# Optimization experiments

Hardware: AMD Instinct MI355X
Metric: run time of the kernel (lower is better)

## Reference

```python
import jax, jax.numpy as jnp
import numpy as np
import math

N_HEAD = 16
STRIDE = 128
C = 8


def _sparse_causal_mask(q_len, k_len):
    # Mirrors LingLongAttention._sparse_causal_mask (static, host-side numpy).
    cols = np.arange(k_len)
    rows = np.arange(k_len)[:, None]
    strided = (cols % STRIDE) >= (STRIDE - C)          # last C cols of each stride block
    local = (cols[None, :] // STRIDE) == (rows // STRIDE)  # same stride block as query
    causal = cols[None, :] <= rows
    layout = (strided[None, :] | local) & causal       # [k_len, k_len]
    return jnp.asarray(layout[k_len - q_len:])         # [q_len, k_len]


def setup_inputs() -> dict:
    key = jax.random.key(0)
    k1, k2, k3 = jax.random.split(key, 3)
    B, S, E = 2, 2048, 1024
    return {
        "hidden_states": jax.random.normal(k1, (B, S, E), dtype=jnp.float32),
        "W_attn": jax.random.normal(k2, (E, 3 * E), dtype=jnp.float32) * 0.02,
        "b_attn": jnp.zeros((3 * E,), dtype=jnp.float32),
        "W_proj": jax.random.normal(k3, (E, E), dtype=jnp.float32) * 0.02,
        "b_proj": jnp.zeros((E,), dtype=jnp.float32),
    }


def reference(hidden_states, W_attn, b_attn, W_proj, b_proj):
    B, S, E = hidden_states.shape
    H = N_HEAD
    D = E // H
    # Conv1D: x @ W + b, then split into q,k,v
    qkv = hidden_states @ W_attn + b_attn                 # [B,S,3E]
    q, k, v = jnp.split(qkv, 3, axis=-1)
    split = lambda t: t.reshape(B, S, H, D).transpose(0, 2, 1, 3)  # [B,H,S,D]
    q, k, v = split(q), split(k), split(v)
    scale = jnp.asarray(1.0 / math.sqrt(D), dtype=q.dtype)
    scores = jnp.einsum("bhqd,bhkd->bhqk", q, k) * scale  # [B,H,S,S]
    mask = _sparse_causal_mask(S, S)[None, None]          # [1,1,S,S]
    mask_value = jnp.asarray(jnp.finfo(scores.dtype).min, dtype=scores.dtype)
    scores = jnp.where(mask, scores, mask_value)
    attn = jax.nn.softmax(scores, axis=-1)
    out = jnp.einsum("bhqk,bhkd->bhqd", attn, v)          # [B,H,S,D]
    out = out.transpose(0, 2, 1, 3).reshape(B, S, E)      # merge heads
    return out @ W_proj + b_proj
```

## Files before the change

kernel.cpp:

```cpp
#include <hip/hip_runtime.h>
#include <hip/hip_bf16.h>
#include <stdint.h>

typedef unsigned short u16;
typedef uint32_t u32;
typedef short s16x8 __attribute__((ext_vector_type(8)));
typedef float f32x4 __attribute__((ext_vector_type(4)));

#define SDIM 2048
#define EDIM 1024

static __device__ __forceinline__ float b2f(u16 v) {
    union { float f; u32 u; } c; c.u = ((u32)v) << 16; return c.f;
}
static __device__ __forceinline__ u16 f2b(float f) {
    union { float f; u32 u; } c; c.f = f;
    u32 u = c.u;
    u32 r = (u + 0x7FFFu + ((u >> 16) & 1u)) >> 16;
    return (u16)r;
}
static __device__ __forceinline__ void gll16(const u16* g, u16* l) {
    __builtin_amdgcn_global_load_lds(
        (const __attribute__((address_space(1))) void*)g,
        (__attribute__((address_space(3))) void*)l, 16, 0, 0);
}

static __device__ __forceinline__ int sniff_bf16(const u16* __restrict__ x) {
    u16 v = x[(threadIdx.x & 63) * 2];
    int e = (v >> 7) & 0xFF;
    unsigned long long m = __ballot(e >= 90 && e <= 144);
    return __popcll(m) >= 48;
}

__global__ __launch_bounds__(256) void k_prep(
    const void* __restrict__ X, const void* __restrict__ Wa,
    const void* __restrict__ Wp, u16* __restrict__ Xb,
    u16* __restrict__ WtA, u16* __restrict__ WtP) {
    int f = sniff_bf16((const u16*)X);
    int z = blockIdx.z;
    int t = threadIdx.x;
    if (z == 2) {
        if (f) return;
        const float* s = (const float*)X;
        int bid = blockIdx.y * 48 + blockIdx.x;
        for (int c = bid; c < 2048; c += 768) {
            long i = ((long)c * 256 + t) * 8;
            u16 o[8];
            for (int j = 0; j < 8; ++j) o[j] = f2b(s[i + j]);
            *(uint4*)&Xb[i] = *(uint4*)o;
        }
        return;
    }
    if (z == 1 && blockIdx.x >= 16) return;
    const void* src = z ? Wp : Wa;
    u16* dst = z ? WtP : WtA;
    int Nsrc = z ? 1024 : 3072;
    int n0 = blockIdx.x * 64, k0 = blockIdx.y * 64;
    __shared__ u16 L[64 * 72];
    int r = t >> 2, c0 = (t & 3) * 16;
    u16 val[16];
    if (f) {
        const u16* s = (const u16*)src + (size_t)(k0 + r) * Nsrc + n0 + c0;
        *(uint4*)&val[0] = *(const uint4*)s;
        *(uint4*)&val[8] = *(const uint4*)(s + 8);
    } else {
        const float* s = (const float*)src + (size_t)(k0 + r) * Nsrc + n0 + c0;
        for (int j = 0; j < 16; ++j) val[j] = f2b(s[j]);
    }
    for (int j = 0; j < 16; ++j) L[(c0 + j) * 72 + r] = val[j];
    __syncthreads();
    uint4 o0 = *(const uint4*)&L[r * 72 + c0];
    uint4 o1 = *(const uint4*)&L[r * 72 + c0 + 8];
    u16* d = dst + (size_t)(n0 + r) * 1024 + k0 + c0;
    *(uint4*)d = o0;
    *(uint4*)(d + 8) = o1;
}

__global__ __launch_bounds__(256) void k_gemm1(
    const u16* __restrict__ Xraw, const u16* __restrict__ Xb,
    const u16* __restrict__ Bt, const void* __restrict__ bias,
    u16* __restrict__ C) {
    const int K = 1024;
    __shared__ u16 As[3][4096];
    __shared__ u16 Bs[3][4096];
    int f = sniff_bf16(Xraw);
    const u16* A = f ? Xraw : Xb;
    int t = threadIdx.x, wave = t >> 6, lane = t & 63;
    int m0 = blockIdx.y * 128, n0 = blockIdx.x * 128;
    int wm = (wave >> 1) * 64, wn = (wave & 1) * 64;
    int lm = lane & 15;
    int lk = (((lane >> 4) ^ ((lane >> 1) & 3))) * 8;
    int sr = t >> 2;
    int sc = ((t & 3) ^ ((t >> 3) & 3)) * 8;
    const u16* Ap = A + (size_t)(m0 + sr) * K + sc;
    const u16* Bp = Bt + (size_t)(n0 + sr) * K + sc;
    int wo = wave * 512;

    f32x4 acc[4][4];
    f32x4 z = {0.f, 0.f, 0.f, 0.f};
    for (int mi = 0; mi < 4; ++mi)
        for (int ni = 0; ni < 4; ++ni) acc[mi][ni] = z;

    gll16(Ap, &As[0][wo]);
    gll16(Ap + (size_t)64 * K, &As[0][wo + 2048]);
    gll16(Bp, &Bs[0][wo]);
    gll16(Bp + (size_t)64 * K, &Bs[0][wo + 2048]);
    gll16(Ap + 32, &As[1][wo]);
    gll16(Ap + (size_t)64 * K + 32, &As[1][wo + 2048]);
    gll16(Bp + 32, &Bs[1][wo]);
    gll16(Bp + (size_t)64 * K + 32, &Bs[1][wo + 2048]);

    u16 *Ac = &As[0][0], *An = &As[1][0], *At = &As[2][0];
    u16 *Bc = &Bs[0][0], *Bn = &Bs[1][0], *Btg = &Bs[2][0];

    for (int it = 0; it < 32; ++it) {
        asm volatile("s_waitcnt vmcnt(4)\n\ts_barrier" ::: "memory");
        int kn = ((it + 2) & 31) * 32;
        gll16(Ap + kn, At + wo);
        gll16(Ap + (size_t)64 * K + kn, At + wo + 2048);
        gll16(Bp + kn, Btg + wo);
        gll16(Bp + (size_t)64 * K + kn, Btg + wo + 2048);

        s16x8 af[4], bfr[4];
        for (int mi = 0; mi < 4; ++mi)
            af[mi] = *(const s16x8*)&Ac[(wm + mi * 16 + lm) * 32 + lk];
        for (int ni = 0; ni < 4; ++ni)
            bfr[ni] = *(const s16x8*)&Bc[(wn + ni * 16 + lm) * 32 + lk];
        for (int mi = 0; mi < 4; ++mi)
            for (int ni = 0; ni < 4; ++ni)
                acc[mi][ni] = __builtin_amdgcn_mfma_f32_16x16x32_bf16(
                    af[mi], bfr[ni], acc[mi][ni], 0, 0, 0);

        u16* tp = Ac; Ac = An; An = At; At = tp;
        tp = Bc; Bc = Bn; Bn = Btg; Btg = tp;
    }
    asm volatile("s_waitcnt vmcnt(0)" ::: "memory");

    int cn = lane & 15, cr = (lane >> 4) * 4;
    for (int ni = 0; ni < 4; ++ni) {
        int gn = n0 + wn + ni * 16 + cn;
        float bb = f ? b2f(((const u16*)bias)[gn]) : ((const float*)bias)[gn];
        int kind = gn >> 10, rem = gn & 1023;
        int h = rem >> 6, d = rem & 63;
        int hm = kind * 32 + h;
        for (int mi = 0; mi < 4; ++mi)
            for (int r = 0; r < 4; ++r) {
                int gm = m0 + wm + mi * 16 + cr + r;
                int b = gm >> 11, s = gm & 2047;
                size_t o = ((size_t)((hm + b * 16) * 2048 + s)) * 64 + d;
                C[o] = f2b(acc[mi][ni][r] + bb);
            }
    }
}

__global__ __launch_bounds__(256) void k_gemm2(
    const u16* __restrict__ Xraw, const u16* __restrict__ A,
    const u16* __restrict__ Bt, const void* __restrict__ bias,
    u16* __restrict__ Cb, float* __restrict__ Cf) {
    const int K = 1024, N = 1024;
    __shared__ u16 As[3][2048];
    __shared__ u16 Bs[3][4096];
    int f = sniff_bf16(Xraw);
    int t = threadIdx.x, wave = t >> 6, lane = t & 63;
    int m0 = blockIdx.y * 64, n0 = blockIdx.x * 128;
    int wm = (wave >> 1) * 32, wn = (wave & 1) * 64;
    int lm = lane & 15;
    int lk = (((lane >> 4) ^ ((lane >> 1) & 3))) * 8;
    int sr = t >> 2;
    int sc = ((t & 3) ^ ((t >> 3) & 3)) * 8;
    const u16* Ap = A + (size_t)(m0 + sr) * K + sc;
    const u16* Bp = Bt + (size_t)(n0 + sr) * K + sc;
    int wo = wave * 512;

    f32x4 acc[2][4];
    f32x4 z = {0.f, 0.f, 0.f, 0.f};
    for (int mi = 0; mi < 2; ++mi)
        for (int ni = 0; ni < 4; ++ni) acc[mi][ni] = z;

    gll16(Ap, &As[0][wo]);
    gll16(Bp, &Bs[0][wo]);
    gll16(Bp + (size_t)64 * K, &Bs[0][wo + 2048]);
    gll16(Ap + 32, &As[1][wo]);
    gll16(Bp + 32, &Bs[1][wo]);
    gll16(Bp + (size_t)64 * K + 32, &Bs[1][wo + 2048]);

    u16 *Ac = &As[0][0], *An = &As[1][0], *At = &As[2][0];
    u16 *Bc = &Bs[0][0], *Bn = &Bs[1][0], *Btg = &Bs[2][0];

    for (int it = 0; it < 32; ++it) {
        asm volatile("s_waitcnt vmcnt(3)\n\ts_barrier" ::: "memory");
        int kn = ((it + 2) & 31) * 32;
        gll16(Ap + kn, At + wo);
        gll16(Bp + kn, Btg + wo);
        gll16(Bp + (size_t)64 * K + kn, Btg + wo + 2048);

        s16x8 af[2], bfr[4];
        for (int mi = 0; mi < 2; ++mi)
            af[mi] = *(const s16x8*)&Ac[(wm + mi * 16 + lm) * 32 + lk];
        for (int ni = 0; ni < 4; ++ni)
            bfr[ni] = *(const s16x8*)&Bc[(wn + ni * 16 + lm) * 32 + lk];
        for (int mi = 0; mi < 2; ++mi)
            for (int ni = 0; ni < 4; ++ni)
                acc[mi][ni] = __builtin_amdgcn_mfma_f32_16x16x32_bf16(
                    af[mi], bfr[ni], acc[mi][ni], 0, 0, 0);

        u16* tp = Ac; Ac = An; An = At; At = tp;
        tp = Bc; Bc = Bn; Bn = Btg; Btg = tp;
    }
    asm volatile("s_waitcnt vmcnt(0)" ::: "memory");

    int store_f32 = (f == 0);
    int cn = lane & 15, cr = (lane >> 4) * 4;
    for (int ni = 0; ni < 4; ++ni) {
        int gn = n0 + wn + ni * 16 + cn;
        float bb = f ? b2f(((const u16*)bias)[gn]) : ((const float*)bias)[gn];
        for (int mi = 0; mi < 2; ++mi)
            for (int r = 0; r < 4; ++r) {
                int gm = m0 + wm + mi * 16 + cr + r;
                float v = acc[mi][ni][r] + bb;
                size_t o = (size_t)gm * N + gn;
                if (store_f32) Cf[o] = v;
                else           Cb[o] = f2b(v);
            }
    }
}

#define VP 264
#define PP 264
__global__ __launch_bounds__(256) void k_attn4(const u16* __restrict__ QKV,
                                               u16* __restrict__ AO) {
    int bx = blockIdx.x, h = blockIdx.y, b = blockIdx.z;
    int qb = bx >> 1, sb = bx & 1;
    int t = threadIdx.x, lane = t & 63, wave = t >> 6;
    int lm = lane & 15, q4 = lane >> 4;
    int nstr = qb << 3;
    int nk = nstr + (sb << 6) + 64;
    int r0 = (qb << 7) + (sb << 6);

    __shared__ char smem[79872];
    u16* Vts = (u16*)smem;
    u16* Qs  = (u16*)(smem + 33792);
    u16* Ks  = (u16*)(smem + 33792 + 9216);
    u16* Ps  = (u16*)(smem + 33792);

    int hm = b * 16 + h;
    const u16* qp = QKV + ((size_t)hm * 2048 + r0) * 64;
    const u16* kp = QKV + ((size_t)(32 + hm) * 2048) * 64;
    const u16* vp = QKV + ((size_t)(64 + hm) * 2048) * 64;

    for (int c = t; c < 512; c += 256) {
        int r = c >> 3, d0 = (c & 7) << 3;
        *(uint4*)&Qs[r * 72 + d0] = *(const uint4*)(qp + c * 8);
    }
    uint4 zz = {0u, 0u, 0u, 0u};
    for (int c = t; c < 2048; c += 256) {
        int i = c >> 3, d0 = (c & 7) << 3;
        uint4 kv = zz;
        if (i < nk) {
            int key = (i < nstr) ? (((i >> 3) << 7) + 120 + (i & 7))
                                 : ((qb << 7) + (i - nstr));
            kv = *(const uint4*)(kp + key * 64 + d0);
        }
        *(uint4*)&Ks[i * 72 + d0] = kv;
    }
    {
        int i0 = (t & 31) * 8, d0 = (t >> 5) * 8;
        u16 m8[8][8];
        for (int r = 0; r < 8; ++r) {
            int i = i0 + r;
            uint4 vv = zz;
            if (i < nk) {
                int key = (i < nstr) ? (((i >> 3) << 7) + 120 + (i & 7))
                                     : ((qb << 7) + (i - nstr));
                vv = *(const uint4*)(vp + key * 64 + d0);
            }
            *(uint4*)m8[r] = vv;
        }
        for (int j = 0; j < 8; ++j) {
            u16 o[8];
            for (int r = 0; r < 8; ++r) o[r] = m8[r][j];
            *(uint4*)&Vts[(d0 + j) * VP + i0] = *(uint4*)o;
        }
    }
    __syncthreads();

    f32x4 acc[16];
    f32x4 z4 = {0.f, 0.f, 0.f, 0.f};
    for (int ni = 0; ni < 16; ++ni) acc[ni] = z4;
    s16x8 af0 = *(const s16x8*)&Qs[(wave * 16 + lm) * 72 + q4 * 8];
    s16x8 af1 = *(const s16x8*)&Qs[(wave * 16 + lm) * 72 + 32 + q4 * 8];
    for (int ni = 0; ni < 16; ++ni) {
        s16x8 bf0 = *(const s16x8*)&Ks[(ni * 16 + lm) * 72 + q4 * 8];
        s16x8 bf1 = *(const s16x8*)&Ks[(ni * 16 + lm) * 72 + 32 + q4 * 8];
        acc[ni] = __builtin_amdgcn_mfma_f32_16x16x32_bf16(af0, bf0, acc[ni], 0, 0, 0);
        acc[ni] = __builtin_amdgcn_mfma_f32_16x16x32_bf16(af1, bf1, acc[ni], 0, 0, 0);
    }
    __syncthreads();

    float mx[4] = {-3e38f, -3e38f, -3e38f, -3e38f};
    for (int ni = 0; ni < 16; ++ni) {
        int i = ni * 16 + lm;
        for (int reg = 0; reg < 4; ++reg) {
            int rl = (sb << 6) + wave * 16 + q4 * 4 + reg;
            bool valid = (i < nstr) || ((i - nstr) <= rl);
            float v = valid ? acc[ni][reg] * 0.125f : -3e38f;
            acc[ni][reg] = v;
            mx[reg] = fmaxf(mx[reg], v);
        }
    }
    for (int reg = 0; reg < 4; ++reg)
        for (int off = 1; off < 16; off <<= 1)
            mx[reg] = fmaxf(mx[reg], __shfl_xor(mx[reg], off, 64));
    float sm[4] = {0.f, 0.f, 0.f, 0.f};
    for (int ni = 0; ni < 16; ++ni)
        for (int reg = 0; reg < 4; ++reg) {
            float e = __expf(acc[ni][reg] - mx[reg]);
            acc[ni][reg] = e;
            sm[reg] += e;
        }
    for (int reg = 0; reg < 4; ++reg)
        for (int off = 1; off < 16; off <<= 1)
            sm[reg] += __shfl_xor(sm[reg], off, 64);
    float inv[4];
    for (int reg = 0; reg < 4; ++reg) inv[reg] = 1.f / sm[reg];

    for (int ni = 0; ni < 16; ++ni) {
        int i = ni * 16 + lm;
        for (int reg = 0; reg < 4; ++reg)
            Ps[(wave * 16 + q4 * 4 + reg) * PP + i] = f2b(acc[ni][reg]);
    }
    __syncthreads();

    f32x4 acc2[4];
    for (int ni2 = 0; ni2 < 4; ++ni2) acc2[ni2] = z4;
    for (int k0 = 0; k0 < 256; k0 += 32) {
        s16x8 pf = *(const s16x8*)&Ps[(wave * 16 + lm) * PP + k0 + q4 * 8];
        for (int ni2 = 0; ni2 < 4; ++ni2) {
            s16x8 vf = *(const s16x8*)&Vts[(ni2 * 16 + lm) * VP + k0 + q4 * 8];
            acc2[ni2] = __builtin_amdgcn_mfma_f32_16x16x32_bf16(pf, vf, acc2[ni2], 0, 0, 0);
        }
    }
    int srow = r0 + wave * 16 + q4 * 4;
    for (int ni2 = 0; ni2 < 4; ++ni2)
        for (int reg = 0; reg < 4; ++reg) {
            size_t o = ((size_t)(b * SDIM + srow + reg)) * EDIM + h * 64 + ni2 * 16 + lm;
            AO[o] = f2b(acc2[ni2][reg] * inv[reg]);
        }
}

extern "C" void kernel_launch(void* const* d_in, const int* in_sizes, int n_in,
                              void* d_out, int out_size, void* d_ws, size_t ws_size,
                              hipStream_t stream) {
    const void* X  = d_in[0];
    const void* Wa = d_in[1];
    const void* ba = d_in[2];
    const void* Wp = d_in[3];
    const void* bp = d_in[4];

    char* w = (char*)d_ws;
    u16* Xb   = (u16*)(w);
    u16* WtA  = (u16*)(w + 8388608);
    u16* WtP  = (u16*)(w + 14680064);
    u16* QKVh = (u16*)(w + 16777216);
    u16* AO   = (u16*)(w + 41943040);

    k_prep<<<dim3(48, 16, 3), 256, 0, stream>>>(X, Wa, Wp, Xb, WtA, WtP);
    k_gemm1<<<dim3(24, 32), 256, 0, stream>>>((const u16*)X, Xb, WtA, ba, QKVh);
    k_attn4<<<dim3(32, 16, 2), 256, 0, stream>>>(QKVh, AO);
    k_gemm2<<<dim3(8, 64), 256, 0, stream>>>((const u16*)X, AO, WtP, bp,
                                             (u16*)d_out, (float*)d_out);
}
```

Before: 163.6 us.

## Rewrite QKV GEMM with 256x256 tiles, 8 waves, and interleaved load/MFMA phases

The QKV projection GEMM moves from 128x128 tiles with 4 waves and a triple-buffered K=32 pipeline to 256x256 tiles with 8 waves and a double-buffered K=64 pipeline. Each iteration is split into four barrier-separated MFMA quadrants, with global-to-LDS loads issued between them and s_setprio raised around the MFMA blocks. A swizzled 1D block index is added for L2 locality. The larger tile is meant to raise data reuse per LDS byte and hide memory latency, but it launches only 192 blocks, which may underfill the CUs, and the 8x4 accumulator array increases register pressure.

```diff
diff --git a/kernel.cpp b/kernel.cpp
--- a/kernel.cpp
+++ b/kernel.cpp
@@ -76,76 +76,151 @@
     *(uint4*)(d + 8) = o1;
 }
 
-__global__ __launch_bounds__(256) void k_gemm1(
+#define G1_STA(h, Tn) do {                                                     \
+    int ko_ = ((Tn) & 15) * 64;                                                \
+    gll16(Ab + (size_t)((h) * 128) * 1024 + ko_,                               \
+          &As[(Tn) & 1][(((h) * 128) + wave * 16) * 64]);                      \
+    gll16(Ab + (size_t)((h) * 128 + 8) * 1024 + ko_,                           \
+          &As[(Tn) & 1][(((h) * 128) + wave * 16 + 8) * 64]);                  \
+} while (0)
+#define G1_STB(h, Tn) do {                                                     \
+    int ko_ = ((Tn) & 15) * 64;                                                \
+    gll16(Bb + (size_t)((h) * 128) * 1024 + ko_,                               \
+          &Bs[(Tn) & 1][(((h) * 128) + wave * 16) * 64]);                      \
+    gll16(Bb + (size_t)((h) * 128 + 8) * 1024 + ko_,                           \
+          &Bs[(Tn) & 1][(((h) * 128) + wave * 16 + 8) * 64]);                  \
+} while (0)
+
+__global__ __launch_bounds__(512, 2) void k_gemm1(
     const u16* __restrict__ Xraw, const u16* __restrict__ Xb,
     const u16* __restrict__ Bt, const void* __restrict__ bias,
     u16* __restrict__ C) {
     const int K = 1024;
-    __shared__ u16 As[3][4096];
-    __shared__ u16 Bs[3][4096];
+    __shared__ u16 As[2][256 * 64];
+    __shared__ u16 Bs[2][256 * 64];
     int f = sniff_bf16(Xraw);
     const u16* A = f ? Xraw : Xb;
     int t = threadIdx.x, wave = t >> 6, lane = t & 63;
-    int m0 = blockIdx.y * 128, n0 = blockIdx.x * 128;
-    int wm = (wave >> 1) * 64, wn = (wave & 1) * 64;
-    int lm = lane & 15;
-    int lk = (((lane >> 4) ^ ((lane >> 1) & 3))) * 8;
-    int sr = t >> 2;
-    int sc = ((t & 3) ^ ((t >> 3) & 3)) * 8;
-    const u16* Ap = A + (size_t)(m0 + sr) * K + sc;
-    const u16* Bp = Bt + (size_t)(n0 + sr) * K + sc;
-    int wo = wave * 512;
-
-    f32x4 acc[4][4];
+    int bid = blockIdx.x;
+    int swz = (bid & 7) * 24 + (bid >> 3);
+    int bx = swz % 12, by = swz / 12;
+    int m0 = by * 256, n0 = bx * 256;
+    int wr = wave >> 2, wc = wave & 3;
+    int lm = lane & 15, q4 = lane >> 4;
+    int l8 = lane >> 3, l7 = lane & 7;
+    int scol = (l7 ^ l8) * 8;
+    const u16* Ab = A  + (size_t)(m0 + wave * 16 + l8) * K + scol;
+    const u16* Bb = Bt + (size_t)(n0 + wave * 16 + l8) * K + scol;
+    int kc0 = ((q4) ^ (lm & 7)) * 8;
+    int kc1 = ((4 + q4) ^ (lm & 7)) * 8;
+
+    f32x4 acc[8][4];
     f32x4 z = {0.f, 0.f, 0.f, 0.f};
-    for (int mi = 0; mi < 4; ++mi)
+#pragma unroll
+    for (int mi = 0; mi < 8; ++mi)
+#pragma unroll
         for (int ni = 0; ni < 4; ++ni) acc[mi][ni] = z;
 
-    gll16(Ap, &As[0][wo]);
-    gll16(Ap + (size_t)64 * K, &As[0][wo + 2048]);
-    gll16(Bp, &Bs[0][wo]);
-    gll16(Bp + (size_t)64 * K, &Bs[0][wo + 2048]);
-    gll16(Ap + 32, &As[1][wo]);
-    gll16(Ap + (size_t)64 * K + 32, &As[1][wo + 2048]);
-    gll16(Bp + 32, &Bs[1][wo]);
-    gll16(Bp + (size_t)64 * K + 32, &Bs[1][wo + 2048]);
-
-    u16 *Ac = &As[0][0], *An = &As[1][0], *At = &As[2][0];
-    u16 *Bc = &Bs[0][0], *Bn = &Bs[1][0], *Btg = &Bs[2][0];
-
-    for (int it = 0; it < 32; ++it) {
+    G1_STA(0, 0); G1_STA(1, 0);
+    G1_STB(0, 0); G1_STB(1, 0);
+    G1_STA(0, 1); G1_STA(1, 1);
+
+    s16x8 afr[8][2], bfr[4][2];
+
+    for (int T = 0; T < 16; ++T) {
+        int p = T & 1;
         asm volatile("s_waitcnt vmcnt(4)\n\ts_barrier" ::: "memory");
-        int kn = ((it + 2) & 31) * 32;
-        gll16(Ap + kn, At + wo);
-        gll16(Ap + (size_t)64 * K + kn, At + wo + 2048);
-        gll16(Bp + kn, Btg + wo);
-        gll16(Bp + (size_t)64 * K + kn, Btg + wo + 2048);
-
-        s16x8 af[4], bfr[4];
+#pragma unroll
+        for (int mi = 0; mi < 4; ++mi) {
+            int rb = (wr * 128 + mi * 16 + lm) * 64;
+            afr[mi][0] = *(const s16x8*)&As[p][rb + kc0];
+            afr[mi][1] = *(const s16x8*)&As[p][rb + kc1];
+        }
+#pragma unroll
+        for (int ni = 0; ni < 2; ++ni) {
+            int rb = (wc * 64 + ni * 16 + lm) * 64;
+            bfr[ni][0] = *(const s16x8*)&Bs[p][rb + kc0];
+            bfr[ni][1] = *(const s16x8*)&Bs[p][rb + kc1];
+        }
+        G1_STB(0, T + 1);
+        __builtin_amdgcn_s_setprio(1);
+#pragma unroll
         for (int mi = 0; mi < 4; ++mi)
-            af[mi] = *(const s16x8*)&Ac[(wm + mi * 16 + lm) * 32 + lk];
-        for (int ni = 0; ni < 4; ++ni)
-            bfr[ni] = *(const s16x8*)&Bc[(wn + ni * 16 + lm) * 32 + lk];
+#pragma unroll
+            for (int ni = 0; ni < 2; ++ni) {
+                acc[mi][ni] = __builtin_amdgcn_mfma_f32_16x16x32_bf16(
+                    afr[mi][0], bfr[ni][0], acc[mi][ni], 0, 0, 0);
+                acc[mi][ni] = __builtin_amdgcn_mfma_f32_16x16x32_bf16(
+                    afr[mi][1], bfr[ni][1], acc[mi][ni], 0, 0, 0);
+            }
+        __builtin_amdgcn_s_setprio(0);
+        asm volatile("s_barrier" ::: "memory");
+#pragma unroll
+        for (int mi = 4; mi < 8; ++mi) {
+            int rb = (wr * 128 + mi * 16 + lm) * 64;
+            afr[mi][0] = *(const s16x8*)&As[p][rb + kc0];
+            afr[mi][1] = *(const s16x8*)&As[p][rb + kc1];
+        }
+#pragma unroll
+        for (int ni = 2; ni < 4; ++ni) {
+            int rb = (wc * 64 + ni * 16 + lm) * 64;
+            bfr[ni][0] = *(const s16x8*)&Bs[p][rb + kc0];
+            bfr[ni][1] = *(const s16x8*)&Bs[p][rb + kc1];
+        }
+        G1_STB(1, T + 1);
+        __builtin_amdgcn_s_setprio(1);
+#pragma unroll
+        for (int mi = 4; mi < 8; ++mi)
+#pragma unroll
+            for (int ni = 2; ni < 4; ++ni) {
+                acc[mi][ni] = __builtin_amdgcn_mfma_f32_16x16x32_bf16(
+                    afr[mi][0], bfr[ni][0], acc[mi][ni], 0, 0, 0);
+                acc[mi][ni] = __builtin_amdgcn_mfma_f32_16x16x32_bf16(
+                    afr[mi][1], bfr[ni][1], acc[mi][ni], 0, 0, 0);
+            }
+        __builtin_amdgcn_s_setprio(0);
+        asm volatile("s_barrier" ::: "memory");
+        G1_STA(0, T + 2);
+        __builtin_amdgcn_s_setprio(1);
+#pragma unroll
         for (int mi = 0; mi < 4; ++mi)
-            for (int ni = 0; ni < 4; ++ni)
-                acc[mi][ni] = __builtin_amdgcn_mfma_f32_16x16x32_bf16(
-                    af[mi], bfr[ni], acc[mi][ni], 0, 0, 0);
-
-        u16* tp = Ac; Ac = An; An = At; At = tp;
-        tp = Bc; Bc = Bn; Bn = Btg; Btg = tp;
+#pragma unroll
+            for (int ni = 2; ni < 4; ++ni) {
+                acc[mi][ni] = __builtin_amdgcn_mfma_f32_16x16x32_bf16(
+                    afr[mi][0], bfr[ni][0], acc[mi][ni], 0, 0, 0);
+                acc[mi][ni] = __builtin_amdgcn_mfma_f32_16x16x32_bf16(
+                    afr[mi][1], bfr[ni][1], acc[mi][ni], 0, 0, 0);
+            }
+        __builtin_amdgcn_s_setprio(0);
+        asm volatile("s_barrier" ::: "memory");
+        G1_STA(1, T + 2);
+        __builtin_amdgcn_s_setprio(1);
+#pragma unroll
+        for (int mi = 4; mi < 8; ++mi)
+#pragma unroll
+            for (int ni = 0; ni < 2; ++ni) {
+                acc[mi][ni] = __builtin_amdgcn_mfma_f32_16x16x32_bf16(
+                    afr[mi][0], bfr[ni][0], acc[mi][ni], 0, 0, 0);
+                acc[mi][ni] = __builtin_amdgcn_mfma_f32_16x16x32_bf16(
+                    afr[mi][1], bfr[ni][1], acc[mi][ni], 0, 0, 0);
+            }
+        __builtin_amdgcn_s_setprio(0);
+        asm volatile("s_barrier" ::: "memory");
     }
     asm volatile("s_waitcnt vmcnt(0)" ::: "memory");
 
-    int cn = lane & 15, cr = (lane >> 4) * 4;
+    int cn = lane & 15, cr = q4 * 4;
+#pragma unroll
     for (int ni = 0; ni < 4; ++ni) {
-        int gn = n0 + wn + ni * 16 + cn;
+        int gn = n0 + wc * 64 + ni * 16 + cn;
         float bb = f ? b2f(((const u16*)bias)[gn]) : ((const float*)bias)[gn];
         int kind = gn >> 10, rem = gn & 1023;
         int h = rem >> 6, d = rem & 63;
         int hm = kind * 32 + h;
-        for (int mi = 0; mi < 4; ++mi)
+#pragma unroll
+        for (int mi = 0; mi < 8; ++mi)
             for (int r = 0; r < 4; ++r) {
-                int gm = m0 + wm + mi * 16 + cr + r;
+                int gm = m0 + wr * 128 + mi * 16 + cr + r;
                 int b = gm >> 11, s = gm & 2047;
                 size_t o = ((size_t)((hm + b * 16) * 2048 + s)) * 64 + d;
                 C[o] = f2b(acc[mi][ni][r] + bb);
@@ -365,7 +440,7 @@
     u16* AO   = (u16*)(w + 41943040);
 
     k_prep<<<dim3(48, 16, 3), 256, 0, stream>>>(X, Wa, Wp, Xb, WtA, WtP);
-    k_gemm1<<<dim3(24, 32), 256, 0, stream>>>((const u16*)X, Xb, WtA, ba, QKVh);
+    k_gemm1<<<dim3(192), 512, 0, stream>>>((const u16*)X, Xb, WtA, ba, QKVh);
     k_attn4<<<dim3(32, 16, 2), 256, 0, stream>>>(QKVh, AO);
     k_gemm2<<<dim3(8, 64), 256, 0, stream>>>((const u16*)X, AO, WtP, bp,
                                              (u16*)d_out, (float*)d_out);
```

New measurement: 162.8 us. About the same (-0.5%).
